# Kernel tuning notes

Hardware: AMD Instinct MI355X
Metric: run time of the kernel (lower is better)

## Reference

```python
import jax, jax.numpy as jnp
import numpy as np

B, C, T, N = 4, 3, 16, 2048

def setup_inputs() -> dict:
    key = jax.random.key(0)
    k1, k2 = jax.random.split(key)
    preds = jax.random.normal(k1, (B, C, T, N), dtype=jnp.float32)
    gts = jax.random.normal(k2, (B, C, T, N), dtype=jnp.float32)
    return {"preds": preds, "gts": gts}

def reference(preds, gts):
    # batch_pairwise_dist(x=gts, y=preds): permute [B,C,T,N] -> [B,T,N,C]
    x = jnp.transpose(gts, (0, 2, 3, 1))   # [B,T,Nx,C]
    y = jnp.transpose(preds, (0, 2, 3, 1))  # [B,T,Ny,C]
    # rx = diag(x x^T), ry = diag(y y^T) == squared norms
    rx = jnp.sum(x * x, axis=-1)  # [B,T,Nx]
    ry = jnp.sum(y * y, axis=-1)  # [B,T,Ny]
    zz = jnp.einsum('btnc,btmc->btnm', x, y)  # [B,T,Nx,Ny]
    P = rx[..., :, None] + ry[..., None, :] - 2.0 * zz  # [B,T,Nx,Ny]
    # min over Nx (dim 2), sum over Ny -> [B,T]
    loss_1 = jnp.sum(jnp.min(P, axis=2), axis=2)
    # min over Ny (dim 3), sum over Nx -> [B,T]
    loss_2 = jnp.sum(jnp.min(P, axis=3), axis=2)
    return jnp.mean(loss_1 + loss_2)
```

## Files before the change

kernel.cpp:

```cpp
#include <hip/hip_runtime.h>
#include <hip/hip_bf16.h>


typedef short short8 __attribute__((ext_vector_type(8)));
typedef float f32x16 __attribute__((ext_vector_type(16)));

#define BV 4
#define CV 3
#define TV 16
#define NV 2048
#define PS (TV * NV)
#define THREADS 256
#define NT 64
#define MPW 4
#define NBLK 512

static __device__ inline short bfh(float v) {
    __hip_bfloat16 h = __float2bfloat16(v);
    return *reinterpret_cast<short*>(&h);
}
static __device__ inline float bff(short s) {
    __hip_bfloat16 h;
    *reinterpret_cast<short*>(&h) = s;
    return __bfloat162float(h);
}
static __device__ inline void split2(float v, short& hi, short& lo) {
    short h = bfh(v);
    hi = h;
    lo = bfh(v - bff(h));
}

__global__ __launch_bounds__(THREADS)
void chamfer_kernel(const float* __restrict__ preds,
                    const float* __restrict__ gts,
                    float* __restrict__ partial)
{
    __shared__ short8 afr[NT * 64];
    __shared__ float red[THREADS / 64];

    const int tid  = threadIdx.x;
    const int lane = tid & 63;
    const int wid  = tid >> 6;
    const int col  = lane & 31;
    const int half = lane >> 5;

    const int blk = blockIdx.x;
    const int q   = blk & 3;
    const int dir = (blk >> 2) & 1;
    const int sl  = blk >> 3;
    const int b   = sl >> 4, t = sl & 15;

    const size_t base = ((size_t)b * CV * TV + t) * NV;
    const float* rsrc = (dir ? preds : gts) + base;
    const float* qsrc = (dir ? gts : preds) + base;

#pragma unroll
    for (int i = 0; i < 8; ++i) {
        int p = tid + THREADS * i;
        float x0 = rsrc[p], x1 = rsrc[PS + p], x2 = rsrc[2 * PS + p];
        float rx = fmaf(x0, x0, fmaf(x1, x1, x2 * x2));
        short sh0, sl0, sh1, sl1, sh2, sl2, rh, rl;
        split2(-2.f * x0, sh0, sl0);
        split2(-2.f * x1, sh1, sl1);
        split2(-2.f * x2, sh2, sl2);
        split2(rx, rh, rl);
        short8 h0, h1;
        h0[0] = sh0; h0[1] = sh1; h0[2] = sh2; h0[3] = sh0;
        h0[4] = sh1; h0[5] = sh2; h0[6] = sl0; h0[7] = sl1;
        h1[0] = sl2; h1[1] = sl0; h1[2] = sl1; h1[3] = sl2;
        h1[4] = rh;  h1[5] = rl;  h1[6] = 0;   h1[7] = 0;
        int slot = (p >> 5) * 64 + (p & 31);
        afr[slot]      = h0;
        afr[slot + 32] = h1;
    }

    short8 bfr[MPW];
    float  ry[MPW];
    const short ONE = 0x3F80;
#pragma unroll
    for (int j = 0; j < MPW; ++j) {
        int mt = q * 16 + wid * 4 + j;
        int m  = mt * 32 + col;
        float y0 = qsrc[m], y1 = qsrc[PS + m], y2 = qsrc[2 * PS + m];
        ry[j] = fmaf(y0, y0, fmaf(y1, y1, y2 * y2));
        short yh0, yl0, yh1, yl1, yh2, yl2;
        split2(y0, yh0, yl0);
        split2(y1, yh1, yl1);
        split2(y2, yh2, yl2);
        short8 f;
        if (half == 0) {
            f[0] = yh0; f[1] = yh1; f[2] = yh2; f[3] = yl0;
            f[4] = yl1; f[5] = yl2; f[6] = yh0; f[7] = yh1;
        } else {
            f[0] = yh2; f[1] = yl0; f[2] = yl1; f[3] = yl2;
            f[4] = ONE; f[5] = ONE; f[6] = 0;   f[7] = 0;
        }
        bfr[j] = f;
    }
    __syncthreads();

    float acc[MPW] = {3.4e38f, 3.4e38f, 3.4e38f, 3.4e38f};
    f32x16 zc = {};
#pragma unroll 4
    for (int nt = 0; nt < NT; ++nt) {
        short8 a = afr[nt * 64 + lane];
#pragma unroll
        for (int j = 0; j < MPW; ++j) {
            f32x16 d = __builtin_amdgcn_mfma_f32_32x32x16_bf16(a, bfr[j], zc, 0, 0, 0);
            float mn = acc[j];
#pragma unroll
            for (int e = 0; e < 16; e += 2)
                mn = fminf(fminf(mn, d[e]), d[e + 1]);
            acc[j] = mn;
        }
    }

    float wsum = 0.f;
#pragma unroll
    for (int j = 0; j < MPW; ++j) {
        float v = acc[j];
        v = fminf(v, __shfl_xor(v, 32, 64));
        wsum += v + ry[j];
    }
#pragma unroll
    for (int o = 32; o > 0; o >>= 1) wsum += __shfl_down(wsum, o, 64);
    if (lane == 0) red[wid] = wsum;
    __syncthreads();
    if (tid == 0)
        partial[blk] = red[0] + red[1] + red[2] + red[3];
}

__global__ __launch_bounds__(THREADS)
void finish_kernel(const float* __restrict__ partial, float* __restrict__ out)
{
    __shared__ float red[THREADS / 64];
    const int tid = threadIdx.x;
    float s = partial[tid] + partial[tid + THREADS];
#pragma unroll
    for (int o = 32; o > 0; o >>= 1) s += __shfl_down(s, o, 64);
    if ((tid & 63) == 0) red[tid >> 6] = s;
    __syncthreads();
    if (tid == 0)
        out[0] = (red[0] + red[1] + red[2] + red[3]) * (1.0f / 128.0f);
}

extern "C" void kernel_launch(void* const* d_in, const int* in_sizes, int n_in,
                              void* d_out, int out_size, void* d_ws, size_t ws_size,
                              hipStream_t stream) {
    const float* preds = (const float*)d_in[0];
    const float* gts   = (const float*)d_in[1];
    float* out = (float*)d_out;
    float* partial = (float*)d_ws;

    chamfer_kernel<<<NBLK, THREADS, 0, stream>>>(preds, gts, partial);
    finish_kernel<<<1, THREADS, 0, stream>>>(partial, out);
}
```

Baseline: 84.47 us.

## Split reference points across two blocks and merge per-query minima in extra pass

Each block now covers half of the reference set, which doubles the grid to 1024 blocks and halves the LDS tile. Each block writes its per-query partial minima to workspace instead of a block sum. A new two-stage finish takes the min across the two halves and then reduces the sums. The aim is better occupancy and CU coverage (launch bounds now request 4 blocks), plus a shorter dependency chain in the min reduction. The cost is an extra kernel launch and global traffic for the partial minima.

```diff
diff --git a/kernel.cpp b/kernel.cpp
--- a/kernel.cpp
+++ b/kernel.cpp
@@ -11,9 +11,11 @@
 #define NV 2048
 #define PS (TV * NV)
 #define THREADS 256
-#define NT 64
+#define NT 32
 #define MPW 4
-#define NBLK 512
+#define NBLK 1024
+#define NCHUNK 512
+#define PQ (NCHUNK * 2 * 512)
 
 static __device__ inline short bfh(float v) {
     __hip_bfloat16 h = __float2bfloat16(v);
@@ -30,13 +32,12 @@
     lo = bfh(v - bff(h));
 }
 
-__global__ __launch_bounds__(THREADS)
+__global__ __launch_bounds__(THREADS, 4)
 void chamfer_kernel(const float* __restrict__ preds,
                     const float* __restrict__ gts,
-                    float* __restrict__ partial)
+                    float* __restrict__ pmin)
 {
     __shared__ short8 afr[NT * 64];
-    __shared__ float red[THREADS / 64];
 
     const int tid  = threadIdx.x;
     const int lane = tid & 63;
@@ -45,9 +46,10 @@
     const int half = lane >> 5;
 
     const int blk = blockIdx.x;
-    const int q   = blk & 3;
-    const int dir = (blk >> 2) & 1;
-    const int sl  = blk >> 3;
+    const int rh  = blk & 1;
+    const int q   = (blk >> 1) & 3;
+    const int dir = (blk >> 3) & 1;
+    const int sl  = blk >> 4;
     const int b   = sl >> 4, t = sl & 15;
 
     const size_t base = ((size_t)b * CV * TV + t) * NV;
@@ -55,20 +57,21 @@
     const float* qsrc = (dir ? gts : preds) + base;
 
 #pragma unroll
-    for (int i = 0; i < 8; ++i) {
-        int p = tid + THREADS * i;
-        float x0 = rsrc[p], x1 = rsrc[PS + p], x2 = rsrc[2 * PS + p];
+    for (int i = 0; i < 4; ++i) {
+        int p  = tid + THREADS * i;
+        int rp = rh * 1024 + p;
+        float x0 = rsrc[rp], x1 = rsrc[PS + rp], x2 = rsrc[2 * PS + rp];
         float rx = fmaf(x0, x0, fmaf(x1, x1, x2 * x2));
-        short sh0, sl0, sh1, sl1, sh2, sl2, rh, rl;
+        short sh0, sl0, sh1, sl1, sh2, sl2, rxh, rxl;
         split2(-2.f * x0, sh0, sl0);
         split2(-2.f * x1, sh1, sl1);
         split2(-2.f * x2, sh2, sl2);
-        split2(rx, rh, rl);
+        split2(rx, rxh, rxl);
         short8 h0, h1;
         h0[0] = sh0; h0[1] = sh1; h0[2] = sh2; h0[3] = sh0;
         h0[4] = sh1; h0[5] = sh2; h0[6] = sl0; h0[7] = sl1;
         h1[0] = sl2; h1[1] = sl0; h1[2] = sl1; h1[3] = sl2;
-        h1[4] = rh;  h1[5] = rl;  h1[6] = 0;   h1[7] = 0;
+        h1[4] = rxh; h1[5] = rxl; h1[6] = 0;   h1[7] = 0;
         int slot = (p >> 5) * 64 + (p & 31);
         afr[slot]      = h0;
         afr[slot + 32] = h1;
@@ -107,41 +110,54 @@
 #pragma unroll
         for (int j = 0; j < MPW; ++j) {
             f32x16 d = __builtin_amdgcn_mfma_f32_32x32x16_bf16(a, bfr[j], zc, 0, 0, 0);
-            float mn = acc[j];
-#pragma unroll
-            for (int e = 0; e < 16; e += 2)
-                mn = fminf(fminf(mn, d[e]), d[e + 1]);
-            acc[j] = mn;
+            float c0 = fminf(fminf(d[0], d[1]), d[2]);
+            c0 = fminf(fminf(c0, d[3]), d[4]);
+            c0 = fminf(fminf(c0, d[5]), d[6]);
+            float c1 = fminf(fminf(d[7], d[8]), d[9]);
+            c1 = fminf(fminf(c1, d[10]), d[11]);
+            c1 = fminf(fminf(c1, d[12]), d[13]);
+            float c2 = fminf(fminf(acc[j], d[14]), d[15]);
+            acc[j] = fminf(fminf(c0, c1), c2);
         }
     }
 
-    float wsum = 0.f;
 #pragma unroll
     for (int j = 0; j < MPW; ++j) {
         float v = acc[j];
         v = fminf(v, __shfl_xor(v, 32, 64));
-        wsum += v + ry[j];
+        if (half == 0)
+            pmin[(size_t)blk * 512 + (wid * 4 + j) * 32 + col] = v + ry[j];
     }
-#pragma unroll
-    for (int o = 32; o > 0; o >>= 1) wsum += __shfl_down(wsum, o, 64);
-    if (lane == 0) red[wid] = wsum;
-    __syncthreads();
-    if (tid == 0)
-        partial[blk] = red[0] + red[1] + red[2] + red[3];
 }
 
 __global__ __launch_bounds__(THREADS)
-void finish_kernel(const float* __restrict__ partial, float* __restrict__ out)
+void finishA_kernel(const float* __restrict__ pmin, float* __restrict__ pb)
 {
     __shared__ float red[THREADS / 64];
     const int tid = threadIdx.x;
-    float s = partial[tid] + partial[tid + THREADS];
+    const int c   = blockIdx.x * 2 + (tid >> 7);
+    const int qi  = (tid & 127) * 4;
+    const float4 a = *(const float4*)(pmin + (size_t)(c * 2) * 512 + qi);
+    const float4 b = *(const float4*)(pmin + (size_t)(c * 2 + 1) * 512 + qi);
+    float s = fminf(a.x, b.x) + fminf(a.y, b.y) + fminf(a.z, b.z) + fminf(a.w, b.w);
 #pragma unroll
     for (int o = 32; o > 0; o >>= 1) s += __shfl_down(s, o, 64);
     if ((tid & 63) == 0) red[tid >> 6] = s;
     __syncthreads();
-    if (tid == 0)
-        out[0] = (red[0] + red[1] + red[2] + red[3]) * (1.0f / 128.0f);
+    if (tid == 0) pb[blockIdx.x] = red[0] + red[1] + red[2] + red[3];
+}
+
+__global__ __launch_bounds__(THREADS)
+void finishB_kernel(const float* __restrict__ pb, float* __restrict__ out)
+{
+    __shared__ float red[THREADS / 64];
+    const int tid = threadIdx.x;
+    float s = pb[tid];
+#pragma unroll
+    for (int o = 32; o > 0; o >>= 1) s += __shfl_down(s, o, 64);
+    if ((tid & 63) == 0) red[tid >> 6] = s;
+    __syncthreads();
+    if (tid == 0) out[0] = (red[0] + red[1] + red[2] + red[3]) * (1.0f / 64.0f);
 }
 
 extern "C" void kernel_launch(void* const* d_in, const int* in_sizes, int n_in,
@@ -149,9 +165,11 @@
                               hipStream_t stream) {
     const float* preds = (const float*)d_in[0];
     const float* gts   = (const float*)d_in[1];
-    float* out = (float*)d_out;
-    float* partial = (float*)d_ws;
+    float* out  = (float*)d_out;
+    float* pmin = (float*)d_ws;
+    float* pb   = pmin + PQ;
 
-    chamfer_kernel<<<NBLK, THREADS, 0, stream>>>(preds, gts, partial);
-    finish_kernel<<<1, THREADS, 0, stream>>>(partial, out);
+    chamfer_kernel<<<NBLK, THREADS, 0, stream>>>(preds, gts, pmin);
+    finishA_kernel<<<256, THREADS, 0, stream>>>(pmin, pb);
+    finishB_kernel<<<1, THREADS, 0, stream>>>(pb, out);
 }
```

New measurement: 75.40 us. 10.7% less time.

## Halve per-wave query tiles, double grid, and repack MFMA operand layout

Applied to the files above, without the earlier changes.

Doubles the grid to 1024 blocks, with each wave covering 2 query tiles instead of 4. The reference fragment is repacked into a single short8 per point that is shared by both lane halves, which halves LDS staging. The hi/lo split terms are redistributed between the A and B operands so that the 16-wide K dimension still computes the full distance. The min reduction now uses a tree-shaped fold to shorten the dependency chain, and the launch bounds request 4 blocks per CU. In exchange, more blocks each redo the reference-fragment preprocessing.

```diff
diff --git a/kernel.cpp b/kernel.cpp
--- a/kernel.cpp
+++ b/kernel.cpp
@@ -12,8 +12,8 @@
 #define PS (TV * NV)
 #define THREADS 256
 #define NT 64
-#define MPW 4
-#define NBLK 512
+#define MPW 2
+#define NBLK 1024
 
 static __device__ inline short bfh(float v) {
     __hip_bfloat16 h = __float2bfloat16(v);
@@ -29,13 +29,23 @@
     hi = h;
     lo = bfh(v - bff(h));
 }
+static __device__ inline float fold16(float accv, const f32x16& d) {
+    float c0 = fminf(fminf(d[0], d[1]), d[2]);
+    c0 = fminf(fminf(c0, d[3]), d[4]);
+    c0 = fminf(fminf(c0, d[5]), d[6]);
+    float c1 = fminf(fminf(d[7], d[8]), d[9]);
+    c1 = fminf(fminf(c1, d[10]), d[11]);
+    c1 = fminf(fminf(c1, d[12]), d[13]);
+    float c2 = fminf(fminf(accv, d[14]), d[15]);
+    return fminf(fminf(c0, c1), c2);
+}
 
-__global__ __launch_bounds__(THREADS)
+__global__ __launch_bounds__(THREADS, 4)
 void chamfer_kernel(const float* __restrict__ preds,
                     const float* __restrict__ gts,
-                    float* __restrict__ partial)
+                    float* __restrict__ pb)
 {
-    __shared__ short8 afr[NT * 64];
+    __shared__ short8 afr[NV];
     __shared__ float red[THREADS / 64];
 
     const int tid  = threadIdx.x;
@@ -45,9 +55,9 @@
     const int half = lane >> 5;
 
     const int blk = blockIdx.x;
-    const int q   = blk & 3;
-    const int dir = (blk >> 2) & 1;
-    const int sl  = blk >> 3;
+    const int qc  = blk & 7;
+    const int dir = (blk >> 3) & 1;
+    const int sl  = blk >> 4;
     const int b   = sl >> 4, t = sl & 15;
 
     const size_t base = ((size_t)b * CV * TV + t) * NV;
@@ -59,19 +69,15 @@
         int p = tid + THREADS * i;
         float x0 = rsrc[p], x1 = rsrc[PS + p], x2 = rsrc[2 * PS + p];
         float rx = fmaf(x0, x0, fmaf(x1, x1, x2 * x2));
-        short sh0, sl0, sh1, sl1, sh2, sl2, rh, rl;
-        split2(-2.f * x0, sh0, sl0);
-        split2(-2.f * x1, sh1, sl1);
-        split2(-2.f * x2, sh2, sl2);
+        short h0, l0, h1, l1, h2, l2, rh, rl;
+        split2(-2.f * x0, h0, l0);
+        split2(-2.f * x1, h1, l1);
+        split2(-2.f * x2, h2, l2);
         split2(rx, rh, rl);
-        short8 h0, h1;
-        h0[0] = sh0; h0[1] = sh1; h0[2] = sh2; h0[3] = sh0;
-        h0[4] = sh1; h0[5] = sh2; h0[6] = sl0; h0[7] = sl1;
-        h1[0] = sl2; h1[1] = sl0; h1[2] = sl1; h1[3] = sl2;
-        h1[4] = rh;  h1[5] = rl;  h1[6] = 0;   h1[7] = 0;
-        int slot = (p >> 5) * 64 + (p & 31);
-        afr[slot]      = h0;
-        afr[slot + 32] = h1;
+        short8 pk;
+        pk[0] = h0; pk[1] = h1; pk[2] = h2; pk[3] = l0;
+        pk[4] = l1; pk[5] = l2; pk[6] = rh; pk[7] = rl;
+        afr[p] = pk;
     }
 
     short8 bfr[MPW];
@@ -79,8 +85,7 @@
     const short ONE = 0x3F80;
 #pragma unroll
     for (int j = 0; j < MPW; ++j) {
-        int mt = q * 16 + wid * 4 + j;
-        int m  = mt * 32 + col;
+        int m = qc * 256 + (wid * MPW + j) * 32 + col;
         float y0 = qsrc[m], y1 = qsrc[PS + m], y2 = qsrc[2 * PS + m];
         ry[j] = fmaf(y0, y0, fmaf(y1, y1, y2 * y2));
         short yh0, yl0, yh1, yl1, yh2, yl2;
@@ -89,29 +94,25 @@
         split2(y2, yh2, yl2);
         short8 f;
         if (half == 0) {
-            f[0] = yh0; f[1] = yh1; f[2] = yh2; f[3] = yl0;
-            f[4] = yl1; f[5] = yl2; f[6] = yh0; f[7] = yh1;
+            f[0] = yh0; f[1] = yh1; f[2] = yh2; f[3] = yh0;
+            f[4] = yh1; f[5] = yh2; f[6] = ONE; f[7] = ONE;
         } else {
-            f[0] = yh2; f[1] = yl0; f[2] = yl1; f[3] = yl2;
-            f[4] = ONE; f[5] = ONE; f[6] = 0;   f[7] = 0;
+            f[0] = yl0; f[1] = yl1; f[2] = yl2; f[3] = yl0;
+            f[4] = yl1; f[5] = yl2; f[6] = 0;   f[7] = 0;
         }
         bfr[j] = f;
     }
     __syncthreads();
 
-    float acc[MPW] = {3.4e38f, 3.4e38f, 3.4e38f, 3.4e38f};
+    float acc[MPW] = {3.4e38f, 3.4e38f};
     f32x16 zc = {};
 #pragma unroll 4
     for (int nt = 0; nt < NT; ++nt) {
-        short8 a = afr[nt * 64 + lane];
+        short8 a = afr[nt * 32 + col];
 #pragma unroll
         for (int j = 0; j < MPW; ++j) {
             f32x16 d = __builtin_amdgcn_mfma_f32_32x32x16_bf16(a, bfr[j], zc, 0, 0, 0);
-            float mn = acc[j];
-#pragma unroll
-            for (int e = 0; e < 16; e += 2)
-                mn = fminf(fminf(mn, d[e]), d[e + 1]);
-            acc[j] = mn;
+            acc[j] = fold16(acc[j], d);
         }
     }
 
@@ -127,15 +128,16 @@
     if (lane == 0) red[wid] = wsum;
     __syncthreads();
     if (tid == 0)
-        partial[blk] = red[0] + red[1] + red[2] + red[3];
+        pb[blk] = red[0] + red[1] + red[2] + red[3];
 }
 
 __global__ __launch_bounds__(THREADS)
-void finish_kernel(const float* __restrict__ partial, float* __restrict__ out)
+void finish_kernel(const float* __restrict__ pb, float* __restrict__ out)
 {
     __shared__ float red[THREADS / 64];
     const int tid = threadIdx.x;
-    float s = partial[tid] + partial[tid + THREADS];
+    const float4 v = *(const float4*)(pb + tid * 4);
+    float s = (v.x + v.y) + (v.z + v.w);
 #pragma unroll
     for (int o = 32; o > 0; o >>= 1) s += __shfl_down(s, o, 64);
     if ((tid & 63) == 0) red[tid >> 6] = s;
@@ -150,8 +152,8 @@
     const float* preds = (const float*)d_in[0];
     const float* gts   = (const float*)d_in[1];
     float* out = (float*)d_out;
-    float* partial = (float*)d_ws;
+    float* pb  = (float*)d_ws;
 
-    chamfer_kernel<<<NBLK, THREADS, 0, stream>>>(preds, gts, partial);
-    finish_kernel<<<1, THREADS, 0, stream>>>(partial, out);
+    chamfer_kernel<<<NBLK, THREADS, 0, stream>>>(preds, gts, pb);
+    finish_kernel<<<1, THREADS, 0, stream>>>(pb, out);
 }
```

Result: faster. 77.37 us (-8.4%).
